# Kernel optimization log

Hardware: AMD Instinct MI355X
Metric: run time of the kernel (lower is better)

The kernel has to match this reference:

```python
import jax, jax.numpy as jnp
import numpy as np

B, S, V, E, H = 256, 64, 30000, 300, 512
D_A, R, C, P = 350, 8, 150, 16
NUM_ITERS = 3
EPS = 1e-9


def _xavier(k, shape, fi, fo):
    lim = (6.0 / (fi + fo)) ** 0.5
    return jax.random.uniform(k, shape, minval=-lim, maxval=lim, dtype=jnp.float32)


def setup_inputs() -> dict:
    key = jax.random.key(0)
    ks = jax.random.split(key, 14)
    u = 1.0 / (H ** 0.5)
    uni = lambda k, shp: jax.random.uniform(k, shp, minval=-u, maxval=u, dtype=jnp.float32)
    return {
        'input_x': jax.random.randint(ks[0], (B, S), 0, V, dtype=jnp.int32),
        'lens': jnp.full((B,), S, dtype=jnp.int32),
        'embedding': jax.random.normal(ks[1], (V, E), dtype=jnp.float32) * 0.1,
        'w_ih_f': uni(ks[2], (4 * H, E)), 'w_hh_f': uni(ks[3], (4 * H, H)),
        'b_ih_f': uni(ks[4], (4 * H,)), 'b_hh_f': uni(ks[5], (4 * H,)),
        'w_ih_b': uni(ks[6], (4 * H, E)), 'w_hh_b': uni(ks[7], (4 * H, H)),
        'b_ih_b': uni(ks[8], (4 * H,)), 'b_hh_b': uni(ks[9], (4 * H,)),
        'ws1': _xavier(ks[10], (D_A, 2 * H), 2 * H, D_A),
        'ws2': _xavier(ks[11], (R, D_A), D_A, R),
        'capsule_weights': _xavier(ks[12], (R, 2 * H, C * P), 2 * H, C * P),
    }


def _lstm_dir(x, w_ih, w_hh, b_ih, b_hh, reverse):
    # x: [S, B, E] -> hidden states [S, B, H] (torch gate order i, f, g, o)
    b = x.shape[1]
    def step(carry, xt):
        h, c = carry
        z = xt @ w_ih.T + h @ w_hh.T + (b_ih + b_hh)
        i, f, g, o = jnp.split(z, 4, axis=-1)
        c = jax.nn.sigmoid(f) * c + jax.nn.sigmoid(i) * jnp.tanh(g)
        h = jax.nn.sigmoid(o) * jnp.tanh(c)
        return (h, c), h
    init = (jnp.zeros((b, H), x.dtype), jnp.zeros((b, H), x.dtype))
    _, hs = jax.lax.scan(step, init, x, reverse=reverse)
    return hs


def _squash(s):
    # tool.squash: (|s|^2 / (1+|s|^2)) * s / |s|
    n2 = jnp.sum(s * s, axis=-1, keepdims=True)
    return (n2 / (1.0 + n2)) * s / jnp.sqrt(n2 + EPS)


def _forward(input_x, embedding, w_ih_f, w_hh_f, b_ih_f, b_hh_f,
             w_ih_b, w_hh_b, b_ih_b, b_hh_b, ws1, ws2, capsule_weights):
    # embed; torch transposes [B,S] -> [S,B] then embeds -> [S,B,E]
    emb = embedding[input_x.T]
    # bidirectional LSTM (lens == S, so pack/pad is identity)
    h_fwd = _lstm_dir(emb, w_ih_f, w_hh_f, b_ih_f, b_hh_f, reverse=False)
    h_bwd = _lstm_dir(emb, w_ih_b, w_hh_b, b_ih_b, b_hh_b, reverse=True)
    output = jnp.transpose(jnp.concatenate([h_fwd, h_bwd], axis=-1), (1, 0, 2))  # [B,S,2H]
    # structured self-attention (dropout is identity at p=0 / eval)
    pre = jnp.tanh(jnp.einsum('bsd,ad->bsa', output, ws1))          # [B,S,d_a]
    att = jnp.einsum('bsa,ra->brs', pre, ws2)                        # [B,r,S]
    attention = jax.nn.softmax(att, axis=-1)
    semantic = jnp.einsum('brs,bsd->brd', attention, output)         # [B,r,2H]
    # prediction vectors: sum_d semantic[b,r,d] * W[r,d,k]
    pred = jnp.einsum('brd,rdk->brk', semantic, capsule_weights)
    pred = pred.reshape(-1, R, C, P)                                 # [B,r,C,P]
    # dynamic routing
    logits = jnp.zeros((pred.shape[0], R, C), pred.dtype)
    routes = None
    v = None
    for _ in range(NUM_ITERS):
        routes = jax.nn.softmax(logits, axis=2)                      # [B,r,C]
        preact = jnp.einsum('brc,brcp->bcp', routes, pred)           # [B,C,P]
        v = _squash(preact)
        logits = logits + jnp.einsum('brcp,bcp->brc', pred, v)
    class_logits = jnp.linalg.norm(v, axis=-1)                       # [B,C]
    return attention, class_logits, pred, routes


def reference(input_x, lens, embedding, w_ih_f, w_hh_f, b_ih_f, b_hh_f,
              w_ih_b, w_hh_b, b_ih_b, b_hh_b, ws1, ws2, capsule_weights):
    del lens  # all lengths == S: pack/pad identity
    return _forward(input_x, embedding, w_ih_f, w_hh_f, b_ih_f, b_hh_f,
                    w_ih_b, w_hh_b, b_ih_b, b_hh_b, ws1, ws2, capsule_weights)
```

## Files before the change

kernel.cpp:

```cpp
#include <hip/hip_runtime.h>
#include <hip/hip_bf16.h>
#include <hip/hip_cooperative_groups.h>
#include <math.h>

#define BB 256
#define SS 64
#define EE 300
#define EPX 320
#define KP 832
#define VV 30000
#define HH 512
#define H2 1024
#define DA 350
#define RR 8
#define CC 150
#define PP 16
#define CP 2400
#define NFLAG (SS * 2 * 4)

#define ATT_OFF    0L
#define CL_OFF     131072L
#define PRED_OFF   169472L
#define ROUTES_OFF 5084672L

typedef _Float16 f16;
typedef f16  f16x8 __attribute__((ext_vector_type(8)));
typedef f16  f16x4 __attribute__((ext_vector_type(4)));
typedef float f32x4 __attribute__((ext_vector_type(4)));

static __device__ __forceinline__ float sigmG(float x) { return 1.0f / (1.0f + expf(-x)); }

__global__ __launch_bounds__(256) void g_gather(
    const int* __restrict__ ids, const float* __restrict__ emb, f16* __restrict__ X16)
{
    const long idx = (long)blockIdx.x * 256 + threadIdx.x;
    if (idx >= (long)SS * BB * EPX) return;
    const int e = (int)(idx % EPX);
    const int row = (int)(idx / EPX);
    const int s = row >> 8, b = row & 255;
    int tok = ids[(long)b * SS + s];
    if ((unsigned)tok >= (unsigned)VV) tok = 0;
    X16[idx] = (e < EE) ? (f16)emb[(long)tok * EE + e] : (f16)0.0f;
}

__global__ __launch_bounds__(256) void g_packw(
    const float* __restrict__ wihF, const float* __restrict__ whhF,
    const float* __restrict__ wihB, const float* __restrict__ whhB,
    f16* __restrict__ W16)
{
    const long idx = (long)blockIdx.x * 256 + threadIdx.x;
    if (idx >= (long)2 * 2048 * KP) return;
    const int dir = (int)(idx / (2048 * KP));
    const int rem = (int)(idx % (2048 * KP));
    const int j = rem / KP, k = rem % KP;
    const float* wih = dir ? wihB : wihF;
    const float* whh = dir ? whhB : whhF;
    float v;
    if (k < EE)        v = wih[(long)j * EE + k];
    else if (k < EPX)  v = 0.0f;
    else               v = whh[(long)j * HH + (k - EPX)];
    W16[idx] = (f16)v;
}

__global__ __launch_bounds__(256) void g_packws1(
    const float* __restrict__ ws1, f16* __restrict__ w)
{
    const int idx = blockIdx.x * 256 + threadIdx.x;
    if (idx >= 384 * 1024) return;
    const int j = idx >> 10;
    w[idx] = (j < DA) ? (f16)ws1[idx] : (f16)0.0f;
}

__global__ __launch_bounds__(256) void g_packcapsT(
    const float* __restrict__ caps, f16* __restrict__ capsT)
{
    __shared__ float t[32][33];
    const int r = blockIdx.z, k0 = blockIdx.x * 32, n0 = blockIdx.y * 32;
    const int tx = threadIdx.x & 31, ty = threadIdx.x >> 5;
    #pragma unroll
    for (int p = 0; p < 4; ++p) {
        const int k = k0 + ty + p * 8;
        const int n = n0 + tx;
        t[ty + p * 8][tx] = (n < CP) ? caps[((long)r * H2 + k) * CP + n] : 0.0f;
    }
    __syncthreads();
    #pragma unroll
    for (int p = 0; p < 4; ++p) {
        const int n = n0 + ty + p * 8;
        if (n < 2432)
            capsT[((long)r * 2432 + n) * H2 + k0 + tx] = (f16)t[tx][ty + p * 8];
    }
}

__global__ __launch_bounds__(512) void g_zeroflags(unsigned* __restrict__ flags)
{
    if (threadIdx.x < NFLAG) flags[threadIdx.x] = 0u;
}

__global__ __launch_bounds__(512, 1) void p_lstm3(
    const f16* __restrict__ X16, f16* __restrict__ hs16,
    f16* __restrict__ hx, unsigned* __restrict__ flags,
    const f16* __restrict__ W16,
    const float* __restrict__ bihF, const float* __restrict__ bhhF,
    const float* __restrict__ bihB, const float* __restrict__ bhhB)
{
    __shared__ f16 Wl[4 * 26 * 64 * 8];
    __shared__ f32x4 part[4][64][4];
    __shared__ f16 hstage[64][16];

    const int bid = blockIdx.x;
    const int dir = bid & 1;
    const int bq  = (bid >> 1) & 3;
    const int ut  = bid >> 3;
    const int u0  = ut * 16;
    const int b0  = bq * 64;
    const int tid = threadIdx.x;
    const int wave = tid >> 6, lane = tid & 63;
    const int bt = wave & 3, kh = wave >> 2;
    const int l15 = lane & 15;
    const int kgrp = (lane >> 4) * 8;

    {
        const f16* Wsrc = W16 + (long)dir * 2048 * KP;
        for (int f = tid; f < 4 * 26 * 64; f += 512) {
            const int g  = f / (26 * 64);
            const int rm = f % (26 * 64);
            const int kt = rm >> 6, ln = rm & 63;
            const long src = ((long)g * HH + u0 + (ln & 15)) * KP + kt * 32 + ((ln >> 4) * 8);
            *(f16x8*)(Wl + (long)f * 8) = *(const f16x8*)(Wsrc + src);
        }
    }
    __syncthreads();

    const int arow = b0 + bt * 16 + l15;
    const int u = u0 + l15;
    const float* bi = dir ? bihB : bihF;
    const float* bh = dir ? bhhB : bhhF;
    const float bias0 = bi[u]          + bh[u];
    const float bias1 = bi[HH + u]     + bh[HH + u];
    const float bias2 = bi[2 * HH + u] + bh[2 * HH + u];
    const float bias3 = bi[3 * HH + u] + bh[3 * HH + u];
    const int rbase = (lane >> 4) * 4;
    float cc[4] = {0.f, 0.f, 0.f, 0.f};

    f32x4 xacc[4];
    const int xb = kh ? 5 : 0;
    auto computeX = [&](int se) {
        #pragma unroll
        for (int g = 0; g < 4; ++g) xacc[g] = (f32x4){0.f, 0.f, 0.f, 0.f};
        const f16* Xrow = X16 + ((long)se * BB + arow) * EPX;
        #pragma unroll
        for (int j = 0; j < 5; ++j) {
            const int kt = xb + j;
            const int k0 = kt * 32 + kgrp;
            const f16x8 afr = *(const f16x8*)(Xrow + k0);
            #pragma unroll
            for (int g = 0; g < 4; ++g) {
                const f16x8 bfr = *(const f16x8*)(Wl + (((g * 26 + kt) << 6) + lane) * 8);
                xacc[g] = __builtin_amdgcn_mfma_f32_16x16x32_f16(afr, bfr, xacc[g], 0, 0, 0);
            }
        }
    };
    computeX(dir ? (SS - 1) : 0);

    const int hb = kh ? 8 : 0;
    for (int s = 0; s < SS; ++s) {
        const int s_eff = dir ? (SS - 1 - s) : s;

        if (s > 0) {
            if (tid == 0) {
                const int fi = ((s - 1) * 2 + dir) * 4 + bq;
                int guard = 0;
                while (__hip_atomic_load(&flags[fi], __ATOMIC_RELAXED,
                                         __HIP_MEMORY_SCOPE_AGENT) < 32u) {
                    __builtin_amdgcn_s_sleep(1);
                    if (++guard > (1 << 22)) break;
                }
            }
            __syncthreads();
        }

        f32x4 acc[4];
        #pragma unroll
        for (int g = 0; g < 4; ++g) acc[g] = xacc[g];

        if (s > 0) {
            const f16* hrow = hx + ((((long)((s - 1) & 1) * 2 + dir) * BB) + arow) * HH;
            #pragma unroll
            for (int j = 0; j < 8; ++j) {
                const int kt = 10 + hb + j;
                const int hk = (hb + j) * 32 + kgrp;
                union { unsigned long long q[2]; f16x8 v; } uu;
                const unsigned long long* hp = (const unsigned long long*)(hrow + hk);
                uu.q[0] = __hip_atomic_load(hp,     __ATOMIC_RELAXED, __HIP_MEMORY_SCOPE_AGENT);
                uu.q[1] = __hip_atomic_load(hp + 1, __ATOMIC_RELAXED, __HIP_MEMORY_SCOPE_AGENT);
                #pragma unroll
                for (int g = 0; g < 4; ++g) {
                    const f16x8 bfr = *(const f16x8*)(Wl + (((g * 26 + kt) << 6) + lane) * 8);
                    acc[g] = __builtin_amdgcn_mfma_f32_16x16x32_f16(uu.v, bfr, acc[g], 0, 0, 0);
                }
            }
        }

        if (kh == 1) {
            #pragma unroll
            for (int g = 0; g < 4; ++g) part[bt][lane][g] = acc[g];
        }
        __syncthreads();
        if (kh == 0) {
            #pragma unroll
            for (int g = 0; g < 4; ++g) acc[g] += part[bt][lane][g];
            #pragma unroll
            for (int i = 0; i < 4; ++i) {
                const int b = b0 + bt * 16 + rbase + i;
                const float zi = acc[0][i] + bias0;
                const float zf = acc[1][i] + bias1;
                const float zg = acc[2][i] + bias2;
                const float zo = acc[3][i] + bias3;
                cc[i] = sigmG(zf) * cc[i] + sigmG(zi) * tanhf(zg);
                const float hv = sigmG(zo) * tanhf(cc[i]);
                hs16[((long)b * SS + s_eff) * H2 + dir * HH + u] = (f16)hv;
                hstage[bt * 16 + rbase + i][l15] = (f16)hv;
            }
        }
        __syncthreads();

        {
            f16* hxw = hx + (((long)(s & 1) * 2 + dir) * BB) * HH;
            if (tid < 256) {
                const int row = tid >> 2, ch = tid & 3;
                union { unsigned long long q; f16 h4[4]; } pk;
                pk.h4[0] = hstage[row][ch * 4 + 0];
                pk.h4[1] = hstage[row][ch * 4 + 1];
                pk.h4[2] = hstage[row][ch * 4 + 2];
                pk.h4[3] = hstage[row][ch * 4 + 3];
                __hip_atomic_store(
                    (unsigned long long*)(hxw + (long)(b0 + row) * HH + u0 + ch * 4),
                    pk.q, __ATOMIC_RELAXED, __HIP_MEMORY_SCOPE_AGENT);
            }
            asm volatile("s_waitcnt vmcnt(0)" ::: "memory");
        }
        __syncthreads();
        if (tid == 0)
            __hip_atomic_fetch_add(&flags[(s * 2 + dir) * 4 + bq], 1u,
                                   __ATOMIC_RELAXED, __HIP_MEMORY_SCOPE_AGENT);

        if (s + 1 < SS) computeX(dir ? (SS - 2 - s) : (s + 1));
    }
}

__global__ __launch_bounds__(256) void g_preG(
    const f16* __restrict__ hs16, const f16* __restrict__ ws1_16,
    f16* __restrict__ pre16)
{
    const int n0 = blockIdx.x * 192;
    const int m0 = blockIdx.y * 64;
    const int tid = threadIdx.x;
    const int wave = tid >> 6, lane = tid & 63;
    const int l15 = lane & 15;
    const int kgrp = (lane >> 4) * 8;
    const f16* Arow = hs16 + (long)(m0 + wave * 16 + l15) * H2;

    f32x4 acc[12];
    #pragma unroll
    for (int nt = 0; nt < 12; ++nt) acc[nt] = (f32x4){0.f, 0.f, 0.f, 0.f};

    for (int kt = 0; kt < 32; ++kt) {
        const int k0 = kt * 32 + kgrp;
        const f16x8 afr = *(const f16x8*)(Arow + k0);
        #pragma unroll
        for (int nt = 0; nt < 12; ++nt) {
            const f16x8 bfr = *(const f16x8*)(ws1_16 + (long)(n0 + nt * 16 + l15) * H2 + k0);
            acc[nt] = __builtin_amdgcn_mfma_f32_16x16x32_f16(afr, bfr, acc[nt], 0, 0, 0);
        }
    }

    const int rbase = (lane >> 4) * 4;
    #pragma unroll
    for (int nt = 0; nt < 12; ++nt) {
        const int n = n0 + nt * 16 + l15;
        if (n < DA) {
            #pragma unroll
            for (int i = 0; i < 4; ++i) {
                const int m = m0 + wave * 16 + rbase + i;
                pre16[(long)m * DA + n] = (f16)tanhf(acc[nt][i]);
            }
        }
    }
}

__global__ __launch_bounds__(512) void g_predG(
    const f16* __restrict__ sem16, const f16* __restrict__ capsT16,
    float* __restrict__ pred_out)
{
    const int n0 = blockIdx.x * 64;
    const int r  = blockIdx.y;
    const int tid = threadIdx.x;
    const int wave = tid >> 6, lane = tid & 63;
    const int l15 = lane & 15;
    const int kgrp = (lane >> 4) * 8;
    const f16* Bp = capsT16 + (long)r * 2432 * H2;
    const f16* A0 = sem16 + ((long)(wave * 32 + l15) * RR + r) * H2;

    f32x4 acc[2][4];
    #pragma unroll
    for (int mt = 0; mt < 2; ++mt)
        #pragma unroll
        for (int nt = 0; nt < 4; ++nt) acc[mt][nt] = (f32x4){0.f, 0.f, 0.f, 0.f};

    for (int kt = 0; kt < 32; ++kt) {
        const int k0 = kt * 32 + kgrp;
        const f16x8 a0 = *(const f16x8*)(A0 + k0);
        const f16x8 a1 = *(const f16x8*)(A0 + (long)16 * RR * H2 + k0);
        #pragma unroll
        for (int nt = 0; nt < 4; ++nt) {
            const f16x8 bfr = *(const f16x8*)(Bp + (long)(n0 + nt * 16 + l15) * H2 + k0);
            acc[0][nt] = __builtin_amdgcn_mfma_f32_16x16x32_f16(a0, bfr, acc[0][nt], 0, 0, 0);
            acc[1][nt] = __builtin_amdgcn_mfma_f32_16x16x32_f16(a1, bfr, acc[1][nt], 0, 0, 0);
        }
    }

    const int rbase = (lane >> 4) * 4;
    #pragma unroll
    for (int mt = 0; mt < 2; ++mt) {
        #pragma unroll
        for (int nt = 0; nt < 4; ++nt) {
            const int n = n0 + nt * 16 + l15;
            if (n < CP) {
                #pragma unroll
                for (int i = 0; i < 4; ++i) {
                    const int m = wave * 32 + mt * 16 + rbase + i;
                    pred_out[((long)m * RR + r) * CP + n] = acc[mt][nt][i];
                }
            }
        }
    }
}

__global__ __launch_bounds__(256) void g_attlog(
    const f16* __restrict__ pre16, const float* __restrict__ ws2,
    float* __restrict__ attlog)
{
    const int idx = blockIdx.x * 256 + threadIdx.x;
    if (idx >= BB * RR * SS) return;
    const int s = idx & 63, r = (idx >> 6) & 7, b = idx >> 9;
    const f16* p = pre16 + ((long)b * SS + s) * DA;
    const float* w = ws2 + (long)r * DA;
    float acc = 0.0f;
    for (int a = 0; a < DA; ++a) acc = fmaf((float)p[a], w[a], acc);
    attlog[idx] = acc;
}

__global__ __launch_bounds__(256) void g_soft(
    const float* __restrict__ attlog, float* __restrict__ att_out)
{
    const int idx = blockIdx.x * 256 + threadIdx.x;
    if (idx >= BB * RR) return;
    const float* L = attlog + (long)idx * SS;
    float mx = L[0];
    for (int s = 1; s < SS; ++s) mx = fmaxf(mx, L[s]);
    float sm = 0.0f;
    for (int s = 0; s < SS; ++s) sm += expf(L[s] - mx);
    for (int s = 0; s < SS; ++s)
        att_out[(long)idx * SS + s] = expf(L[s] - mx) / sm;
}

__global__ __launch_bounds__(256) void g_sem(
    const float* __restrict__ att, const f16* __restrict__ hs16,
    f16* __restrict__ sem16)
{
    __shared__ float aS[RR * SS];
    const int b = blockIdx.x, tid = threadIdx.x;
    for (int i = tid; i < RR * SS; i += 256) aS[i] = att[(long)b * RR * SS + i];
    __syncthreads();
    const int d0 = tid * 4;
    float acc[RR][4] = {};
    const f16* hb = hs16 + (long)b * SS * H2;
    for (int s = 0; s < SS; ++s) {
        const f16x4 hv = *(const f16x4*)(hb + s * H2 + d0);
        const float h0 = hv[0], h1 = hv[1], h2 = hv[2], h3 = hv[3];
        #pragma unroll
        for (int r = 0; r < RR; ++r) {
            const float a = aS[r * SS + s];
            acc[r][0] = fmaf(a, h0, acc[r][0]);
            acc[r][1] = fmaf(a, h1, acc[r][1]);
            acc[r][2] = fmaf(a, h2, acc[r][2]);
            acc[r][3] = fmaf(a, h3, acc[r][3]);
        }
    }
    #pragma unroll
    for (int r = 0; r < RR; ++r) {
        f16x4 o; o[0] = (f16)acc[r][0]; o[1] = (f16)acc[r][1];
        o[2] = (f16)acc[r][2]; o[3] = (f16)acc[r][3];
        *(f16x4*)(sem16 + ((long)b * RR + r) * H2 + d0) = o;
    }
}

__global__ __launch_bounds__(256) void g_route(
    const float* __restrict__ pred,
    float* __restrict__ cls_out, float* __restrict__ routes_out)
{
    __shared__ float predS[RR * CP];
    __shared__ float logitS[RR * CC];
    __shared__ float routeS[RR * CC];
    __shared__ float preactS[CP];
    __shared__ float vS[CP];
    __shared__ float scaleS[CC];
    __shared__ float rmax[RR], rsum[RR];
    const int b = blockIdx.x, tid = threadIdx.x;
    const float* ps = pred + (long)b * RR * CP;
    for (int i = tid; i < RR * CP; i += 256) predS[i] = ps[i];
    for (int i = tid; i < RR * CC; i += 256) logitS[i] = 0.0f;
    __syncthreads();

    for (int it = 0; it < 3; ++it) {
        if (tid < RR) {
            float mx = -1e30f;
            for (int c = 0; c < CC; ++c) mx = fmaxf(mx, logitS[tid * CC + c]);
            float sm = 0.0f;
            for (int c = 0; c < CC; ++c) sm += expf(logitS[tid * CC + c] - mx);
            rmax[tid] = mx; rsum[tid] = sm;
        }
        __syncthreads();
        for (int i = tid; i < RR * CC; i += 256) {
            const int r = i / CC;
            routeS[i] = expf(logitS[i] - rmax[r]) / rsum[r];
        }
        __syncthreads();
        for (int cp = tid; cp < CP; cp += 256) {
            const int c = cp >> 4;
            float a = 0.0f;
            #pragma unroll
            for (int r = 0; r < RR; ++r)
                a = fmaf(routeS[r * CC + c], predS[r * CP + cp], a);
            preactS[cp] = a;
        }
        __syncthreads();
        for (int c = tid; c < CC; c += 256) {
            float n2 = 0.0f;
            #pragma unroll
            for (int p = 0; p < PP; ++p) { const float x = preactS[c * PP + p]; n2 = fmaf(x, x, n2); }
            scaleS[c] = (n2 / (1.0f + n2)) / sqrtf(n2 + 1e-9f);
        }
        __syncthreads();
        for (int cp = tid; cp < CP; cp += 256) vS[cp] = preactS[cp] * scaleS[cp >> 4];
        __syncthreads();
        for (int i = tid; i < RR * CC; i += 256) {
            const int r = i / CC, c = i % CC;
            float a = 0.0f;
            #pragma unroll
            for (int p = 0; p < PP; ++p)
                a = fmaf(predS[r * CP + c * PP + p], vS[c * PP + p], a);
            logitS[i] += a;
        }
        __syncthreads();
    }

    for (int i = tid; i < RR * CC; i += 256)
        routes_out[(long)b * RR * CC + i] = routeS[i];
    for (int c = tid; c < CC; c += 256) {
        float n2 = 0.0f;
        #pragma unroll
        for (int p = 0; p < PP; ++p) { const float x = vS[c * PP + p]; n2 = fmaf(x, x, n2); }
        cls_out[(long)b * CC + c] = sqrtf(n2);
    }
}

extern "C" void kernel_launch(void* const* d_in, const int* in_sizes, int n_in,
                              void* d_out, int out_size, void* d_ws, size_t ws_size,
                              hipStream_t stream)
{
    (void)in_sizes; (void)n_in; (void)out_size;
    const int*   ids   = (const int*)d_in[0];
    const float* emb   = (const float*)d_in[2];
    const float* wih_f = (const float*)d_in[3];
    const float* whh_f = (const float*)d_in[4];
    const float* bih_f = (const float*)d_in[5];
    const float* bhh_f = (const float*)d_in[6];
    const float* wih_b = (const float*)d_in[7];
    const float* whh_b = (const float*)d_in[8];
    const float* bih_b = (const float*)d_in[9];
    const float* bhh_b = (const float*)d_in[10];
    const float* ws1   = (const float*)d_in[11];
    const float* ws2   = (const float*)d_in[12];
    const float* caps  = (const float*)d_in[13];
    float* out = (float*)d_out;

    float* ws = (float*)d_ws;
    f16*  hs16   = (f16*)ws;
    f16*  hx     = (f16*)(ws + 8388608);
    f16*  X16    = (f16*)(ws + 8650752);
    f16*  W16    = (f16*)(ws + 11272192);
    f16*  ws1_16 = (f16*)(ws + 12976128);
    f16*  sem16  = (f16*)(ws + 13172736);
    float* attlog = ws + 14221312;
    unsigned* flags = (unsigned*)(ws + 14352384);
    f16*  pre16  = X16;
    f16*  capsT16 = (f16*)ws;
    const size_t need = (size_t)(14352384 + 512) * 4;
    if (ws_size < need) return;

    g_gather<<<(int)(((long)SS * BB * EPX + 255) / 256), 256, 0, stream>>>(ids, emb, X16);
    g_packw<<<(int)(((long)2 * 2048 * KP + 255) / 256), 256, 0, stream>>>(
        wih_f, whh_f, wih_b, whh_b, W16);
    g_packws1<<<(384 * 1024) / 256, 256, 0, stream>>>(ws1, ws1_16);
    g_zeroflags<<<1, 512, 0, stream>>>(flags);

    {
        const f16* a0 = X16; f16* a1 = hs16; f16* a2 = hx; unsigned* a3 = flags;
        const f16* a4 = W16;
        const float* a5 = bih_f; const float* a6 = bhh_f;
        const float* a7 = bih_b; const float* a8 = bhh_b;
        void* kargs[] = {(void*)&a0, (void*)&a1, (void*)&a2, (void*)&a3, (void*)&a4,
                         (void*)&a5, (void*)&a6, (void*)&a7, (void*)&a8};
        hipLaunchCooperativeKernel((void*)p_lstm3, dim3(256), dim3(512),
                                   kargs, 0, stream);
    }

    g_preG<<<dim3(2, 256), 256, 0, stream>>>(hs16, ws1_16, pre16);

    g_attlog<<<512, 256, 0, stream>>>(pre16, ws2, attlog);
    g_soft<<<8, 256, 0, stream>>>(attlog, out + ATT_OFF);
    g_sem<<<BB, 256, 0, stream>>>(out + ATT_OFF, hs16, sem16);

    g_packcapsT<<<dim3(32, 76, 8), 256, 0, stream>>>(caps, capsT16);

    g_predG<<<dim3(38, 8), 512, 0, stream>>>(sem16, capsT16, out + PRED_OFF);

    g_route<<<BB, 256, 0, stream>>>(out + PRED_OFF, out + CL_OFF, out + ROUTES_OFF);
}
```

Baseline: 862.9 us.

## Per-wave LSTM step sync, merge staging kernels, fuse attention logits and softmax

In the persistent LSTM kernel, each output wave now publishes its own h slice and increments the step flag itself, with the consumer waiting for 128 wave arrivals. This replaces block-wide barriers and a single-thread signal, shortening the serial critical path of each timestep. The gather, weight pack, ws1 pack and flag-zeroing kernels are merged into one launch, and attention logits plus softmax become one per-batch kernel followed by a device copy. Dropping the barrier after the flag wait relies on lane-0 spinning in each wave. That may weaken the ordering of the cross-block h loads.

```diff
diff --git a/kernel.cpp b/kernel.cpp
--- a/kernel.cpp
+++ b/kernel.cpp
@@ -28,50 +28,49 @@
 typedef f16  f16x4 __attribute__((ext_vector_type(4)));
 typedef float f32x4 __attribute__((ext_vector_type(4)));
 
-static __device__ __forceinline__ float sigmG(float x) { return 1.0f / (1.0f + expf(-x)); }
-
-__global__ __launch_bounds__(256) void g_gather(
-    const int* __restrict__ ids, const float* __restrict__ emb, f16* __restrict__ X16)
-{
-    const long idx = (long)blockIdx.x * 256 + threadIdx.x;
-    if (idx >= (long)SS * BB * EPX) return;
-    const int e = (int)(idx % EPX);
-    const int row = (int)(idx / EPX);
-    const int s = row >> 8, b = row & 255;
-    int tok = ids[(long)b * SS + s];
-    if ((unsigned)tok >= (unsigned)VV) tok = 0;
-    X16[idx] = (e < EE) ? (f16)emb[(long)tok * EE + e] : (f16)0.0f;
-}
-
-__global__ __launch_bounds__(256) void g_packw(
+static __device__ __forceinline__ float sigmH(float x) { return 1.0f / (1.0f + expf(-x)); }
+
+#define NG_ ((long)SS * BB * EPX)
+#define NW_ ((long)2 * 2048 * KP)
+#define NS_ ((long)384 * 1024)
+__global__ __launch_bounds__(256) void h_stage(
+    const int* __restrict__ ids, const float* __restrict__ emb,
     const float* __restrict__ wihF, const float* __restrict__ whhF,
     const float* __restrict__ wihB, const float* __restrict__ whhB,
-    f16* __restrict__ W16)
+    const float* __restrict__ ws1,
+    f16* __restrict__ X16, f16* __restrict__ W16, f16* __restrict__ ws1_16,
+    unsigned* __restrict__ flags)
 {
     const long idx = (long)blockIdx.x * 256 + threadIdx.x;
-    if (idx >= (long)2 * 2048 * KP) return;
-    const int dir = (int)(idx / (2048 * KP));
-    const int rem = (int)(idx % (2048 * KP));
-    const int j = rem / KP, k = rem % KP;
-    const float* wih = dir ? wihB : wihF;
-    const float* whh = dir ? whhB : whhF;
-    float v;
-    if (k < EE)        v = wih[(long)j * EE + k];
-    else if (k < EPX)  v = 0.0f;
-    else               v = whh[(long)j * HH + (k - EPX)];
-    W16[idx] = (f16)v;
-}
-
-__global__ __launch_bounds__(256) void g_packws1(
-    const float* __restrict__ ws1, f16* __restrict__ w)
-{
-    const int idx = blockIdx.x * 256 + threadIdx.x;
-    if (idx >= 384 * 1024) return;
-    const int j = idx >> 10;
-    w[idx] = (j < DA) ? (f16)ws1[idx] : (f16)0.0f;
-}
-
-__global__ __launch_bounds__(256) void g_packcapsT(
+    if (idx < NG_) {
+        const int e = (int)(idx % EPX);
+        const int row = (int)(idx / EPX);
+        const int s = row >> 8, b = row & 255;
+        int tok = ids[(long)b * SS + s];
+        if ((unsigned)tok >= (unsigned)VV) tok = 0;
+        X16[idx] = (e < EE) ? (f16)emb[(long)tok * EE + e] : (f16)0.0f;
+    } else if (idx < NG_ + NW_) {
+        const long i2 = idx - NG_;
+        const int dir = (int)(i2 / (2048 * KP));
+        const int rem = (int)(i2 % (2048 * KP));
+        const int j = rem / KP, k = rem % KP;
+        const float* wih = dir ? wihB : wihF;
+        const float* whh = dir ? whhB : whhF;
+        float v;
+        if (k < EE)        v = wih[(long)j * EE + k];
+        else if (k < EPX)  v = 0.0f;
+        else               v = whh[(long)j * HH + (k - EPX)];
+        W16[i2] = (f16)v;
+    } else if (idx < NG_ + NW_ + NS_) {
+        const long i3 = idx - NG_ - NW_;
+        const int j = (int)(i3 >> 10);
+        ws1_16[i3] = (j < DA) ? (f16)ws1[i3] : (f16)0.0f;
+    } else if (idx < NG_ + NW_ + NS_ + NFLAG) {
+        flags[idx - NG_ - NW_ - NS_] = 0u;
+    }
+}
+
+__global__ __launch_bounds__(256) void h_packcapsT(
     const float* __restrict__ caps, f16* __restrict__ capsT)
 {
     __shared__ float t[32][33];
@@ -92,12 +91,7 @@
     }
 }
 
-__global__ __launch_bounds__(512) void g_zeroflags(unsigned* __restrict__ flags)
-{
-    if (threadIdx.x < NFLAG) flags[threadIdx.x] = 0u;
-}
-
-__global__ __launch_bounds__(512, 1) void p_lstm3(
+__global__ __launch_bounds__(512, 1) void p_lstm4(
     const f16* __restrict__ X16, f16* __restrict__ hs16,
     f16* __restrict__ hx, unsigned* __restrict__ flags,
     const f16* __restrict__ W16,
@@ -106,7 +100,7 @@
 {
     __shared__ f16 Wl[4 * 26 * 64 * 8];
     __shared__ f32x4 part[4][64][4];
-    __shared__ f16 hstage[64][16];
+    __shared__ f16 hstage[4][16][16];
 
     const int bid = blockIdx.x;
     const int dir = bid & 1;
@@ -168,16 +162,16 @@
         const int s_eff = dir ? (SS - 1 - s) : s;
 
         if (s > 0) {
-            if (tid == 0) {
+            if (lane == 0) {
                 const int fi = ((s - 1) * 2 + dir) * 4 + bq;
                 int guard = 0;
                 while (__hip_atomic_load(&flags[fi], __ATOMIC_RELAXED,
-                                         __HIP_MEMORY_SCOPE_AGENT) < 32u) {
-                    __builtin_amdgcn_s_sleep(1);
+                                         __HIP_MEMORY_SCOPE_AGENT) < 128u) {
+                    __builtin_amdgcn_s_sleep(2);
                     if (++guard > (1 << 22)) break;
                 }
             }
-            __syncthreads();
+            asm volatile("" ::: "memory");
         }
 
         f32x4 acc[4];
@@ -207,49 +201,47 @@
             for (int g = 0; g < 4; ++g) part[bt][lane][g] = acc[g];
         }
         __syncthreads();
+
         if (kh == 0) {
             #pragma unroll
             for (int g = 0; g < 4; ++g) acc[g] += part[bt][lane][g];
             #pragma unroll
             for (int i = 0; i < 4; ++i) {
-                const int b = b0 + bt * 16 + rbase + i;
                 const float zi = acc[0][i] + bias0;
                 const float zf = acc[1][i] + bias1;
                 const float zg = acc[2][i] + bias2;
                 const float zo = acc[3][i] + bias3;
-                cc[i] = sigmG(zf) * cc[i] + sigmG(zi) * tanhf(zg);
-                const float hv = sigmG(zo) * tanhf(cc[i]);
-                hs16[((long)b * SS + s_eff) * H2 + dir * HH + u] = (f16)hv;
-                hstage[bt * 16 + rbase + i][l15] = (f16)hv;
+                cc[i] = sigmH(zf) * cc[i] + sigmH(zi) * tanhf(zg);
+                hstage[bt][rbase + i][l15] = (f16)(sigmH(zo) * tanhf(cc[i]));
             }
-        }
-        __syncthreads();
-
-        {
-            f16* hxw = hx + (((long)(s & 1) * 2 + dir) * BB) * HH;
-            if (tid < 256) {
-                const int row = tid >> 2, ch = tid & 3;
-                union { unsigned long long q; f16 h4[4]; } pk;
-                pk.h4[0] = hstage[row][ch * 4 + 0];
-                pk.h4[1] = hstage[row][ch * 4 + 1];
-                pk.h4[2] = hstage[row][ch * 4 + 2];
-                pk.h4[3] = hstage[row][ch * 4 + 3];
-                __hip_atomic_store(
-                    (unsigned long long*)(hxw + (long)(b0 + row) * HH + u0 + ch * 4),
-                    pk.q, __ATOMIC_RELAXED, __HIP_MEMORY_SCOPE_AGENT);
-            }
+            asm volatile("s_waitcnt lgkmcnt(0)" ::: "memory");
+            __builtin_amdgcn_sched_barrier(0);
+
+            const int row = lane >> 2, ch = lane & 3;
+            union { unsigned long long q; f16 h4[4]; } pk;
+            pk.h4[0] = hstage[bt][row][ch * 4 + 0];
+            pk.h4[1] = hstage[bt][row][ch * 4 + 1];
+            pk.h4[2] = hstage[bt][row][ch * 4 + 2];
+            pk.h4[3] = hstage[bt][row][ch * 4 + 3];
+            const int brow = b0 + bt * 16 + row;
+            __hip_atomic_store(
+                (unsigned long long*)(hx + (((long)(s & 1) * 2 + dir) * BB
+                                            + brow) * HH + u0 + ch * 4),
+                pk.q, __ATOMIC_RELAXED, __HIP_MEMORY_SCOPE_AGENT);
             asm volatile("s_waitcnt vmcnt(0)" ::: "memory");
-        }
-        __syncthreads();
-        if (tid == 0)
-            __hip_atomic_fetch_add(&flags[(s * 2 + dir) * 4 + bq], 1u,
-                                   __ATOMIC_RELAXED, __HIP_MEMORY_SCOPE_AGENT);
+            if (lane == 0)
+                __hip_atomic_fetch_add(&flags[(s * 2 + dir) * 4 + bq], 1u,
+                                       __ATOMIC_RELAXED, __HIP_MEMORY_SCOPE_AGENT);
+
+            *(unsigned long long*)(hs16 + ((long)brow * SS + s_eff) * H2
+                                   + dir * HH + u0 + ch * 4) = pk.q;
+        }
 
         if (s + 1 < SS) computeX(dir ? (SS - 2 - s) : (s + 1));
     }
 }
 
-__global__ __launch_bounds__(256) void g_preG(
+__global__ __launch_bounds__(256) void h_preG(
     const f16* __restrict__ hs16, const f16* __restrict__ ws1_16,
     f16* __restrict__ pre16)
 {
@@ -289,7 +281,78 @@
     }
 }
 
-__global__ __launch_bounds__(512) void g_predG(
+__global__ __launch_bounds__(256) void h_att(
+    const f16* __restrict__ pre16, const float* __restrict__ ws2,
+    float* __restrict__ att_out)
+{
+    __shared__ f16 preS[SS * DA];
+    __shared__ float w2S[RR * DA];
+    __shared__ float logS[RR * SS];
+    __shared__ float rmax[RR], rsum[RR];
+    const int b = blockIdx.x, tid = threadIdx.x;
+    {
+        const unsigned long long* src =
+            (const unsigned long long*)(pre16 + (long)b * SS * DA);
+        unsigned long long* dst = (unsigned long long*)preS;
+        for (int i = tid; i < SS * DA / 4; i += 256) dst[i] = src[i];
+    }
+    for (int i = tid; i < RR * DA; i += 256) w2S[i] = ws2[i];
+    __syncthreads();
+    for (int pp = tid; pp < RR * SS; pp += 256) {
+        const int r = pp >> 6, s = pp & 63;
+        const f16* prow = &preS[s * DA];
+        const float* wrow = &w2S[r * DA];
+        float a = 0.0f;
+        for (int k = 0; k < DA; ++k) a = fmaf((float)prow[k], wrow[k], a);
+        logS[r * SS + s] = a;
+    }
+    __syncthreads();
+    if (tid < RR) {
+        float mx = -1e30f;
+        for (int s = 0; s < SS; ++s) mx = fmaxf(mx, logS[tid * SS + s]);
+        float sm = 0.0f;
+        for (int s = 0; s < SS; ++s) sm += expf(logS[tid * SS + s] - mx);
+        rmax[tid] = mx; rsum[tid] = sm;
+    }
+    __syncthreads();
+    for (int pp = tid; pp < RR * SS; pp += 256) {
+        const int r = pp >> 6;
+        att_out[(long)b * RR * SS + pp] = expf(logS[pp] - rmax[r]) / rsum[r];
+    }
+}
+
+__global__ __launch_bounds__(256) void h_sem(
+    const float* __restrict__ att, const f16* __restrict__ hs16,
+    f16* __restrict__ sem16)
+{
+    __shared__ float aS[RR * SS];
+    const int b = blockIdx.x, tid = threadIdx.x;
+    for (int i = tid; i < RR * SS; i += 256) aS[i] = att[(long)b * RR * SS + i];
+    __syncthreads();
+    const int d0 = tid * 4;
+    float acc[RR][4] = {};
+    const f16* hb = hs16 + (long)b * SS * H2;
+    for (int s = 0; s < SS; ++s) {
+        const f16x4 hv = *(const f16x4*)(hb + s * H2 + d0);
+        const float h0 = hv[0], h1 = hv[1], h2 = hv[2], h3 = hv[3];
+        #pragma unroll
+        for (int r = 0; r < RR; ++r) {
+            const float a = aS[r * SS + s];
+            acc[r][0] = fmaf(a, h0, acc[r][0]);
+            acc[r][1] = fmaf(a, h1, acc[r][1]);
+            acc[r][2] = fmaf(a, h2, acc[r][2]);
+            acc[r][3] = fmaf(a, h3, acc[r][3]);
+        }
+    }
+    #pragma unroll
+    for (int r = 0; r < RR; ++r) {
+        f16x4 o; o[0] = (f16)acc[r][0]; o[1] = (f16)acc[r][1];
+        o[2] = (f16)acc[r][2]; o[3] = (f16)acc[r][3];
+        *(f16x4*)(sem16 + ((long)b * RR + r) * H2 + d0) = o;
+    }
+}
+
+__global__ __launch_bounds__(512) void h_predG(
     const f16* __restrict__ sem16, const f16* __restrict__ capsT16,
     float* __restrict__ pred_out)
 {
@@ -337,66 +400,7 @@
     }
 }
 
-__global__ __launch_bounds__(256) void g_attlog(
-    const f16* __restrict__ pre16, const float* __restrict__ ws2,
-    float* __restrict__ attlog)
-{
-    const int idx = blockIdx.x * 256 + threadIdx.x;
-    if (idx >= BB * RR * SS) return;
-    const int s = idx & 63, r = (idx >> 6) & 7, b = idx >> 9;
-    const f16* p = pre16 + ((long)b * SS + s) * DA;
-    const float* w = ws2 + (long)r * DA;
-    float acc = 0.0f;
-    for (int a = 0; a < DA; ++a) acc = fmaf((float)p[a], w[a], acc);
-    attlog[idx] = acc;
-}
-
-__global__ __launch_bounds__(256) void g_soft(
-    const float* __restrict__ attlog, float* __restrict__ att_out)
-{
-    const int idx = blockIdx.x * 256 + threadIdx.x;
-    if (idx >= BB * RR) return;
-    const float* L = attlog + (long)idx * SS;
-    float mx = L[0];
-    for (int s = 1; s < SS; ++s) mx = fmaxf(mx, L[s]);
-    float sm = 0.0f;
-    for (int s = 0; s < SS; ++s) sm += expf(L[s] - mx);
-    for (int s = 0; s < SS; ++s)
-        att_out[(long)idx * SS + s] = expf(L[s] - mx) / sm;
-}
-
-__global__ __launch_bounds__(256) void g_sem(
-    const float* __restrict__ att, const f16* __restrict__ hs16,
-    f16* __restrict__ sem16)
-{
-    __shared__ float aS[RR * SS];
-    const int b = blockIdx.x, tid = threadIdx.x;
-    for (int i = tid; i < RR * SS; i += 256) aS[i] = att[(long)b * RR * SS + i];
-    __syncthreads();
-    const int d0 = tid * 4;
-    float acc[RR][4] = {};
-    const f16* hb = hs16 + (long)b * SS * H2;
-    for (int s = 0; s < SS; ++s) {
-        const f16x4 hv = *(const f16x4*)(hb + s * H2 + d0);
-        const float h0 = hv[0], h1 = hv[1], h2 = hv[2], h3 = hv[3];
-        #pragma unroll
-        for (int r = 0; r < RR; ++r) {
-            const float a = aS[r * SS + s];
-            acc[r][0] = fmaf(a, h0, acc[r][0]);
-            acc[r][1] = fmaf(a, h1, acc[r][1]);
-            acc[r][2] = fmaf(a, h2, acc[r][2]);
-            acc[r][3] = fmaf(a, h3, acc[r][3]);
-        }
-    }
-    #pragma unroll
-    for (int r = 0; r < RR; ++r) {
-        f16x4 o; o[0] = (f16)acc[r][0]; o[1] = (f16)acc[r][1];
-        o[2] = (f16)acc[r][2]; o[3] = (f16)acc[r][3];
-        *(f16x4*)(sem16 + ((long)b * RR + r) * H2 + d0) = o;
-    }
-}
-
-__global__ __launch_bounds__(256) void g_route(
+__global__ __launch_bounds__(256) void h_route(
     const float* __restrict__ pred,
     float* __restrict__ cls_out, float* __restrict__ routes_out)
 {
@@ -493,18 +497,18 @@
     f16*  W16    = (f16*)(ws + 11272192);
     f16*  ws1_16 = (f16*)(ws + 12976128);
     f16*  sem16  = (f16*)(ws + 13172736);
-    float* attlog = ws + 14221312;
+    float* attw  = ws + 14221312;
     unsigned* flags = (unsigned*)(ws + 14352384);
     f16*  pre16  = X16;
     f16*  capsT16 = (f16*)ws;
     const size_t need = (size_t)(14352384 + 512) * 4;
     if (ws_size < need) return;
 
-    g_gather<<<(int)(((long)SS * BB * EPX + 255) / 256), 256, 0, stream>>>(ids, emb, X16);
-    g_packw<<<(int)(((long)2 * 2048 * KP + 255) / 256), 256, 0, stream>>>(
-        wih_f, whh_f, wih_b, whh_b, W16);
-    g_packws1<<<(384 * 1024) / 256, 256, 0, stream>>>(ws1, ws1_16);
-    g_zeroflags<<<1, 512, 0, stream>>>(flags);
+    {
+        const long total = NG_ + NW_ + NS_ + NFLAG;
+        h_stage<<<(int)((total + 255) / 256), 256, 0, stream>>>(
+            ids, emb, wih_f, whh_f, wih_b, whh_b, ws1, X16, W16, ws1_16, flags);
+    }
 
     {
         const f16* a0 = X16; f16* a1 = hs16; f16* a2 = hx; unsigned* a3 = flags;
@@ -513,19 +517,21 @@
         const float* a7 = bih_b; const float* a8 = bhh_b;
         void* kargs[] = {(void*)&a0, (void*)&a1, (void*)&a2, (void*)&a3, (void*)&a4,
                          (void*)&a5, (void*)&a6, (void*)&a7, (void*)&a8};
-        hipLaunchCooperativeKernel((void*)p_lstm3, dim3(256), dim3(512),
+        hipLaunchCooperativeKernel((void*)p_lstm4, dim3(256), dim3(512),
                                    kargs, 0, stream);
     }
 
-    g_preG<<<dim3(2, 256), 256, 0, stream>>>(hs16, ws1_16, pre16);
-
-    g_attlog<<<512, 256, 0, stream>>>(pre16, ws2, attlog);
-    g_soft<<<8, 256, 0, stream>>>(attlog, out + ATT_OFF);
-    g_sem<<<BB, 256, 0, stream>>>(out + ATT_OFF, hs16, sem16);
-
-    g_packcapsT<<<dim3(32, 76, 8), 256, 0, stream>>>(caps, capsT16);
-
-    g_predG<<<dim3(38, 8), 512, 0, stream>>>(sem16, capsT16, out + PRED_OFF);
-
-    g_route<<<BB, 256, 0, stream>>>(out + PRED_OFF, out + CL_OFF, out + ROUTES_OFF);
-}
+    h_preG<<<dim3(2, 256), 256, 0, stream>>>(hs16, ws1_16, pre16);
+
+    h_att<<<BB, 256, 0, stream>>>(pre16, ws2, attw);
+    hipMemcpyAsync(out + ATT_OFF, attw, (size_t)BB * RR * SS * 4,
+                   hipMemcpyDeviceToDevice, stream);
+
+    h_sem<<<BB, 256, 0, stream>>>(attw, hs16, sem16);
+
+    h_packcapsT<<<dim3(32, 76, 8), 256, 0, stream>>>(caps, capsT16);
+
+    h_predG<<<dim3(38, 8), 512, 0, stream>>>(sem16, capsT16, out + PRED_OFF);
+
+    h_route<<<BB, 256, 0, stream>>>(out + PRED_OFF, out + CL_OFF, out + ROUTES_OFF);
+}
```

New measurement: 1.645 ms. 90.6% more time.
